# Performance work log

Hardware: AMD Instinct MI355X
Metric: run time of the kernel (lower is better)

## Reference

```python
import jax, jax.numpy as jnp
import numpy as np

B, L, H, HEADS = 4, 256, 256, 4
D = H // HEADS
NEG = jnp.float32(-2.0**32 + 1)


def setup_inputs() -> dict:
    key = jax.random.key(0)
    ks = jax.random.split(key, 16)
    inp = {
        "queries": jax.random.normal(ks[0], (B, L, H), jnp.float32),
        "keys": jax.random.normal(ks[1], (B, L, H), jnp.float32),
        "values": jax.random.normal(ks[2], (B, L, H), jnp.float32),
        "time_matrix_K": jax.random.normal(ks[3], (B, L, L, H), jnp.float32),
        "time_matrix_V": jax.random.normal(ks[4], (B, L, L, H), jnp.float32),
        "abs_pos_K": jax.random.normal(ks[5], (B, L, H), jnp.float32),
        "abs_pos_V": jax.random.normal(ks[6], (B, L, H), jnp.float32),
        "time_mask": jax.random.randint(ks[7], (B, L), 0, 2) == 1,
        "future_time_mask": jnp.triu(jnp.ones((L, L), bool), k=1),
        # linear layer params (torch Linear: y = x @ W.T + b)
        "Wq": jax.random.normal(ks[8], (H, H), jnp.float32) / np.sqrt(H),
        "bq": jax.random.normal(ks[9], (H,), jnp.float32) * 0.01,
        "Wk": jax.random.normal(ks[10], (H, H), jnp.float32) / np.sqrt(H),
        "bk": jax.random.normal(ks[11], (H,), jnp.float32) * 0.01,
        "Wv": jax.random.normal(ks[12], (H, H), jnp.float32) / np.sqrt(H),
        "bv": jax.random.normal(ks[13], (H,), jnp.float32) * 0.01,
    }
    return inp


def _split_heads(x):  # [B,L,H] -> [h,B,L,d]
    b, l, _ = x.shape
    return x.reshape(b, l, HEADS, D).transpose(2, 0, 1, 3)


def _split_heads_rel(t):  # [B,L,L,H] -> [h,B,L,L,d]
    b, l, _, _ = t.shape
    return t.reshape(b, l, l, HEADS, D).transpose(3, 0, 1, 2, 4)


def reference(queries, keys, values, time_matrix_K, time_matrix_V,
              abs_pos_K, abs_pos_V, time_mask, future_time_mask,
              Wq, bq, Wk, bk, Wv, bv):
    Q = _split_heads(queries @ Wq.T + bq)   # [h,B,L,d]
    K = _split_heads(keys @ Wk.T + bk)
    V = _split_heads(values @ Wv.T + bv)
    tK = _split_heads_rel(time_matrix_K)    # [h,B,L,L,d]
    tV = _split_heads_rel(time_matrix_V)
    pK = _split_heads(abs_pos_K)            # [h,B,L,d]
    pV = _split_heads(abs_pos_V)

    scores = jnp.einsum("hbqd,hbkd->hbqk", Q, K)
    scores += jnp.einsum("hbqd,hbkd->hbqk", Q, pK)
    scores += jnp.einsum("hbqkd,hbqd->hbqk", tK, Q)
    scores = scores / jnp.sqrt(jnp.float32(D))

    mask = time_mask[None, :, :, None] | future_time_mask[None, None, :, :]
    scores = jnp.where(mask, NEG, scores)
    attn = jax.nn.softmax(scores, axis=-1)  # [h,B,L,L]  (dropout: eval mode)

    out = jnp.einsum("hbqk,hbkd->hbqd", attn, V)
    out += jnp.einsum("hbqk,hbkd->hbqd", attn, pV)
    out += jnp.einsum("hbqk,hbqkd->hbqd", attn, tV)
    # merge heads: [h,B,L,d] -> [B,L,H]
    return out.transpose(1, 2, 0, 3).reshape(B, L, H)
```

## Files before the change

### kernel.cpp

```cpp
#include <hip/hip_runtime.h>
#include <math.h>
#include <stdint.h>

#define LSEQ 256
#define HD 256

__device__ __forceinline__ float dot4(float4 a, float4 b) {
    return a.x * b.x + a.y * b.y + a.z * b.z + a.w * b.w;
}
__device__ __forceinline__ float4 add4(float4 a, float4 b) {
    return make_float4(a.x + b.x, a.y + b.y, a.z + b.z, a.w + b.w);
}

__global__ __launch_bounds__(256) void proj_kernel(
    const float* __restrict__ queries, const float* __restrict__ keys,
    const float* __restrict__ values,
    const float* __restrict__ apK, const float* __restrict__ apV,
    const float* __restrict__ Wq, const float* __restrict__ bq,
    const float* __restrict__ Wk, const float* __restrict__ bk,
    const float* __restrict__ Wv, const float* __restrict__ bv,
    float* __restrict__ Qo, float* __restrict__ Ko, float* __restrict__ Vo)
{
    const int R = 4;
    int tid = threadIdx.x;
    int row0 = blockIdx.x * R;

    float aq[R] = {0.f, 0.f, 0.f, 0.f};
    float ak[R] = {0.f, 0.f, 0.f, 0.f};
    float av[R] = {0.f, 0.f, 0.f, 0.f};

    const float* wq = Wq + tid * HD;
    const float* wk = Wk + tid * HD;
    const float* wv = Wv + tid * HD;

    #pragma unroll 2
    for (int i = 0; i < HD; i += 4) {
        float4 wq4 = *(const float4*)(wq + i);
        float4 wk4 = *(const float4*)(wk + i);
        float4 wv4 = *(const float4*)(wv + i);
        #pragma unroll
        for (int r = 0; r < R; ++r) {
            float4 xq = *(const float4*)(queries + (row0 + r) * HD + i);
            float4 xk = *(const float4*)(keys    + (row0 + r) * HD + i);
            float4 xv = *(const float4*)(values  + (row0 + r) * HD + i);
            aq[r] += dot4(xq, wq4);
            ak[r] += dot4(xk, wk4);
            av[r] += dot4(xv, wv4);
        }
    }
    #pragma unroll
    for (int r = 0; r < R; ++r) {
        int idx = (row0 + r) * HD + tid;
        Qo[idx] = aq[r] + bq[tid];
        Ko[idx] = ak[r] + bk[tid] + apK[idx];
        Vo[idx] = av[r] + bv[tid] + apV[idx];
    }
}

__global__ __launch_bounds__(256, 4) void scores_kernel(
    const float* __restrict__ Q, const float* __restrict__ Keff,
    const float* __restrict__ tK, const int* __restrict__ tmask,
    float* __restrict__ sc_out)
{
    int bid = blockIdx.x;
    int bq = bid >> 3;
    int c = bid & 7;
    int q = bq & 255;
    int b = bq >> 8;
    int k0c = c << 5;
    if (k0c > q || tmask[bq]) return;

    int tid = threadIdx.x;
    int v = tid >> 6;
    int lane = tid & 63;
    int head = lane >> 4;
    int le4 = lane * 4;

    const float* tKr = tK + (size_t)bq * (LSEQ * HD);
    const float* Kb  = Keff + b * (LSEQ * HD);
    float4 q4 = *(const float4*)(Q + bq * HD + le4);
    int kend = min(k0c + 32, q + 1);
    float* scrow = sc_out + (size_t)(bq * 4 + head) * LSEQ;

    int k = k0c + v;
    for (; k + 12 < kend; k += 16) {
        float4 t0 = *(const float4*)(tKr + (k     ) * HD + le4);
        float4 t1 = *(const float4*)(tKr + (k +  4) * HD + le4);
        float4 t2 = *(const float4*)(tKr + (k +  8) * HD + le4);
        float4 t3 = *(const float4*)(tKr + (k + 12) * HD + le4);
        float4 c0 = *(const float4*)(Kb  + (k     ) * HD + le4);
        float4 c1 = *(const float4*)(Kb  + (k +  4) * HD + le4);
        float4 c2 = *(const float4*)(Kb  + (k +  8) * HD + le4);
        float4 c3 = *(const float4*)(Kb  + (k + 12) * HD + le4);
        float s0 = dot4(q4, add4(t0, c0));
        float s1 = dot4(q4, add4(t1, c1));
        float s2 = dot4(q4, add4(t2, c2));
        float s3 = dot4(q4, add4(t3, c3));
        #pragma unroll
        for (int off = 1; off <= 8; off <<= 1) {
            s0 += __shfl_xor(s0, off);
            s1 += __shfl_xor(s1, off);
            s2 += __shfl_xor(s2, off);
            s3 += __shfl_xor(s3, off);
        }
        if ((lane & 15) == 0) {
            scrow[k     ] = s0 * 0.125f;
            scrow[k +  4] = s1 * 0.125f;
            scrow[k +  8] = s2 * 0.125f;
            scrow[k + 12] = s3 * 0.125f;
        }
    }
    for (; k < kend; k += 4) {
        float4 t0 = *(const float4*)(tKr + k * HD + le4);
        float4 c0 = *(const float4*)(Kb  + k * HD + le4);
        float s0 = dot4(q4, add4(t0, c0));
        #pragma unroll
        for (int off = 1; off <= 8; off <<= 1)
            s0 += __shfl_xor(s0, off);
        if ((lane & 15) == 0) scrow[k] = s0 * 0.125f;
    }
}

__global__ __launch_bounds__(256, 4) void softmax_kernel(
    float* __restrict__ sc, const int* __restrict__ tmask)
{
    int bq = blockIdx.x;
    if (tmask[bq]) return;
    int q = bq & 255;
    int tid = threadIdx.x;
    int w = tid >> 6;
    int lane = tid & 63;
    float* row = sc + (size_t)(bq * 4 + w) * LSEQ;
    int k0 = lane * 4;
    float4 vv = *(const float4*)(row + k0);
    float x0 = (k0 + 0 <= q) ? vv.x : -INFINITY;
    float x1 = (k0 + 1 <= q) ? vv.y : -INFINITY;
    float x2 = (k0 + 2 <= q) ? vv.z : -INFINITY;
    float x3 = (k0 + 3 <= q) ? vv.w : -INFINITY;
    float m = fmaxf(fmaxf(x0, x1), fmaxf(x2, x3));
    #pragma unroll
    for (int off = 32; off >= 1; off >>= 1)
        m = fmaxf(m, __shfl_xor(m, off));
    float e0 = __expf(x0 - m);
    float e1 = __expf(x1 - m);
    float e2 = __expf(x2 - m);
    float e3 = __expf(x3 - m);
    float ssum = e0 + e1 + e2 + e3;
    #pragma unroll
    for (int off = 32; off >= 1; off >>= 1)
        ssum += __shfl_xor(ssum, off);
    float inv = 1.0f / ssum;
    *(float4*)(row + k0) = make_float4(e0 * inv, e1 * inv, e2 * inv, e3 * inv);
}

__global__ __launch_bounds__(256, 4) void pv_kernel(
    const float* __restrict__ Veff, const float* __restrict__ tV,
    const float* __restrict__ attn, const int* __restrict__ tmask,
    float* __restrict__ part)
{
    __shared__ float outp[4][256];

    int bid = blockIdx.x;
    int bq = bid >> 2;
    int c = bid & 3;
    int q = bq & 255;
    int b = bq >> 8;
    bool masked = tmask[bq] != 0;
    int kstart = c << 6;
    if (!masked && kstart > q) return;
    int kend = min(kstart + 64, masked ? LSEQ : q + 1);

    int tid = threadIdx.x;
    int v = tid >> 6;
    int lane = tid & 63;
    int head = lane >> 4;
    int le4 = lane * 4;

    const float* tVr = tV + (size_t)bq * (LSEQ * HD);
    const float* Vb  = Veff + b * (LSEQ * HD);
    const float* arow = attn + (size_t)(bq * 4 + head) * LSEQ;
    const float uw = 1.0f / 256.0f;

    float4 acc = make_float4(0.f, 0.f, 0.f, 0.f);
    int k = kstart + v;
    for (; k + 12 < kend; k += 16) {
        float4 t0 = *(const float4*)(tVr + (k     ) * HD + le4);
        float4 t1 = *(const float4*)(tVr + (k +  4) * HD + le4);
        float4 t2 = *(const float4*)(tVr + (k +  8) * HD + le4);
        float4 t3 = *(const float4*)(tVr + (k + 12) * HD + le4);
        float4 v0 = *(const float4*)(Vb  + (k     ) * HD + le4);
        float4 v1 = *(const float4*)(Vb  + (k +  4) * HD + le4);
        float4 v2 = *(const float4*)(Vb  + (k +  8) * HD + le4);
        float4 v3 = *(const float4*)(Vb  + (k + 12) * HD + le4);
        float a0 = masked ? uw : arow[k     ];
        float a1 = masked ? uw : arow[k +  4];
        float a2 = masked ? uw : arow[k +  8];
        float a3 = masked ? uw : arow[k + 12];
        acc.x += a0 * (t0.x + v0.x) + a1 * (t1.x + v1.x)
               + a2 * (t2.x + v2.x) + a3 * (t3.x + v3.x);
        acc.y += a0 * (t0.y + v0.y) + a1 * (t1.y + v1.y)
               + a2 * (t2.y + v2.y) + a3 * (t3.y + v3.y);
        acc.z += a0 * (t0.z + v0.z) + a1 * (t1.z + v1.z)
               + a2 * (t2.z + v2.z) + a3 * (t3.z + v3.z);
        acc.w += a0 * (t0.w + v0.w) + a1 * (t1.w + v1.w)
               + a2 * (t2.w + v2.w) + a3 * (t3.w + v3.w);
    }
    for (; k < kend; k += 4) {
        float4 t0 = *(const float4*)(tVr + k * HD + le4);
        float4 v0 = *(const float4*)(Vb  + k * HD + le4);
        float a0 = masked ? uw : arow[k];
        acc.x += a0 * (t0.x + v0.x);
        acc.y += a0 * (t0.y + v0.y);
        acc.z += a0 * (t0.z + v0.z);
        acc.w += a0 * (t0.w + v0.w);
    }
    *(float4*)(&outp[v][le4]) = acc;
    __syncthreads();
    float o = outp[0][tid] + outp[1][tid] + outp[2][tid] + outp[3][tid];
    part[((size_t)((c << 10) | bq)) * HD + tid] = o;
}

__global__ __launch_bounds__(256) void reduce_kernel(
    const float* __restrict__ part, const int* __restrict__ tmask,
    float* __restrict__ out)
{
    int bq = blockIdx.x;
    int q = bq & 255;
    int tid = threadIdx.x;
    int nch = tmask[bq] ? 4 : ((q >> 6) + 1);
    float o = 0.f;
    for (int c = 0; c < nch; ++c)
        o += part[((size_t)((c << 10) | bq)) * HD + tid];
    out[(size_t)bq * HD + tid] = o;
}

extern "C" void kernel_launch(void* const* d_in, const int* in_sizes, int n_in,
                              void* d_out, int out_size, void* d_ws, size_t ws_size,
                              hipStream_t stream) {
    const float* queries = (const float*)d_in[0];
    const float* keys    = (const float*)d_in[1];
    const float* values  = (const float*)d_in[2];
    const float* tK      = (const float*)d_in[3];
    const float* tV      = (const float*)d_in[4];
    const float* apK     = (const float*)d_in[5];
    const float* apV     = (const float*)d_in[6];
    const int*   tmask   = (const int*)d_in[7];
    const float* Wq = (const float*)d_in[9];
    const float* bq = (const float*)d_in[10];
    const float* Wk = (const float*)d_in[11];
    const float* bk = (const float*)d_in[12];
    const float* Wv = (const float*)d_in[13];
    const float* bv = (const float*)d_in[14];

    float* ws = (float*)d_ws;
    float* Qo     = ws;
    float* Ko     = ws + 262144;
    float* Vo     = ws + 524288;
    float* scores = ws + 786432;
    float* partb  = ws + 1835008;
    float* out = (float*)d_out;

    proj_kernel<<<256, 256, 0, stream>>>(queries, keys, values, apK, apV,
                                         Wq, bq, Wk, bk, Wv, bv, Qo, Ko, Vo);
    scores_kernel<<<8192, 256, 0, stream>>>(Qo, Ko, tK, tmask, scores);
    softmax_kernel<<<1024, 256, 0, stream>>>(scores, tmask);
    pv_kernel<<<4096, 256, 0, stream>>>(Vo, tV, scores, tmask, partb);
    reduce_kernel<<<1024, 256, 0, stream>>>(partb, tmask, out);
}
```

Measured before the change: 113.5 us.

## Use nontemporal loads for time matrices and contiguous per-wave key ranges

Streams the large tK/tV tensors with nontemporal loads so they do not pollute cache that K/V reuse needs. Each wave now handles a contiguous 16-key range instead of interleaved keys, which allows float4 stores of scores and float4 loads of attention weights. The scores kernel is re-gridded to 64-key chunks with half as many blocks, and the occupancy hints are dropped from the launch bounds. Contiguous ranges may give less even load balance near the causal boundary.

```diff
diff --git a/kernel.cpp b/kernel.cpp
--- a/kernel.cpp
+++ b/kernel.cpp
@@ -5,11 +5,17 @@
 #define LSEQ 256
 #define HD 256
 
+typedef float floatx4 __attribute__((ext_vector_type(4)));
+
 __device__ __forceinline__ float dot4(float4 a, float4 b) {
     return a.x * b.x + a.y * b.y + a.z * b.z + a.w * b.w;
 }
 __device__ __forceinline__ float4 add4(float4 a, float4 b) {
     return make_float4(a.x + b.x, a.y + b.y, a.z + b.z, a.w + b.w);
+}
+__device__ __forceinline__ float4 ldnt4(const float* p) {
+    floatx4 r = __builtin_nontemporal_load((const floatx4*)p);
+    return make_float4(r.x, r.y, r.z, r.w);
 }
 
 __global__ __launch_bounds__(256) void proj_kernel(
@@ -57,17 +63,17 @@
     }
 }
 
-__global__ __launch_bounds__(256, 4) void scores_kernel(
+__global__ __launch_bounds__(256) void scores_kernel(
     const float* __restrict__ Q, const float* __restrict__ Keff,
     const float* __restrict__ tK, const int* __restrict__ tmask,
     float* __restrict__ sc_out)
 {
     int bid = blockIdx.x;
-    int bq = bid >> 3;
-    int c = bid & 7;
+    int bq = bid >> 2;
+    int c = bid & 3;
     int q = bq & 255;
     int b = bq >> 8;
-    int k0c = c << 5;
+    int k0c = c << 6;
     if (k0c > q || tmask[bq]) return;
 
     int tid = threadIdx.x;
@@ -79,19 +85,21 @@
     const float* tKr = tK + (size_t)bq * (LSEQ * HD);
     const float* Kb  = Keff + b * (LSEQ * HD);
     float4 q4 = *(const float4*)(Q + bq * HD + le4);
-    int kend = min(k0c + 32, q + 1);
     float* scrow = sc_out + (size_t)(bq * 4 + head) * LSEQ;
 
-    int k = k0c + v;
-    for (; k + 12 < kend; k += 16) {
-        float4 t0 = *(const float4*)(tKr + (k     ) * HD + le4);
-        float4 t1 = *(const float4*)(tKr + (k +  4) * HD + le4);
-        float4 t2 = *(const float4*)(tKr + (k +  8) * HD + le4);
-        float4 t3 = *(const float4*)(tKr + (k + 12) * HD + le4);
-        float4 c0 = *(const float4*)(Kb  + (k     ) * HD + le4);
-        float4 c1 = *(const float4*)(Kb  + (k +  4) * HD + le4);
-        float4 c2 = *(const float4*)(Kb  + (k +  8) * HD + le4);
-        float4 c3 = *(const float4*)(Kb  + (k + 12) * HD + le4);
+    int r0 = k0c + v * 16;
+    int rend = min(r0 + 16, q + 1);
+
+    int k = r0;
+    for (; k + 3 < rend; k += 4) {
+        float4 t0 = ldnt4(tKr + (k    ) * HD + le4);
+        float4 t1 = ldnt4(tKr + (k + 1) * HD + le4);
+        float4 t2 = ldnt4(tKr + (k + 2) * HD + le4);
+        float4 t3 = ldnt4(tKr + (k + 3) * HD + le4);
+        float4 c0 = *(const float4*)(Kb + (k    ) * HD + le4);
+        float4 c1 = *(const float4*)(Kb + (k + 1) * HD + le4);
+        float4 c2 = *(const float4*)(Kb + (k + 2) * HD + le4);
+        float4 c3 = *(const float4*)(Kb + (k + 3) * HD + le4);
         float s0 = dot4(q4, add4(t0, c0));
         float s1 = dot4(q4, add4(t1, c1));
         float s2 = dot4(q4, add4(t2, c2));
@@ -103,16 +111,13 @@
             s2 += __shfl_xor(s2, off);
             s3 += __shfl_xor(s3, off);
         }
-        if ((lane & 15) == 0) {
-            scrow[k     ] = s0 * 0.125f;
-            scrow[k +  4] = s1 * 0.125f;
-            scrow[k +  8] = s2 * 0.125f;
-            scrow[k + 12] = s3 * 0.125f;
-        }
-    }
-    for (; k < kend; k += 4) {
-        float4 t0 = *(const float4*)(tKr + k * HD + le4);
-        float4 c0 = *(const float4*)(Kb  + k * HD + le4);
+        if ((lane & 15) == 0)
+            *(float4*)(scrow + k) = make_float4(s0 * 0.125f, s1 * 0.125f,
+                                                s2 * 0.125f, s3 * 0.125f);
+    }
+    for (; k < rend; ++k) {
+        float4 t0 = ldnt4(tKr + k * HD + le4);
+        float4 c0 = *(const float4*)(Kb + k * HD + le4);
         float s0 = dot4(q4, add4(t0, c0));
         #pragma unroll
         for (int off = 1; off <= 8; off <<= 1)
@@ -121,7 +126,7 @@
     }
 }
 
-__global__ __launch_bounds__(256, 4) void softmax_kernel(
+__global__ __launch_bounds__(256) void softmax_kernel(
     float* __restrict__ sc, const int* __restrict__ tmask)
 {
     int bq = blockIdx.x;
@@ -153,7 +158,7 @@
     *(float4*)(row + k0) = make_float4(e0 * inv, e1 * inv, e2 * inv, e3 * inv);
 }
 
-__global__ __launch_bounds__(256, 4) void pv_kernel(
+__global__ __launch_bounds__(256) void pv_kernel(
     const float* __restrict__ Veff, const float* __restrict__ tV,
     const float* __restrict__ attn, const int* __restrict__ tmask,
     float* __restrict__ part)
@@ -168,7 +173,7 @@
     bool masked = tmask[bq] != 0;
     int kstart = c << 6;
     if (!masked && kstart > q) return;
-    int kend = min(kstart + 64, masked ? LSEQ : q + 1);
+    int kendc = min(kstart + 64, masked ? LSEQ : q + 1);
 
     int tid = threadIdx.x;
     int v = tid >> 6;
@@ -181,33 +186,35 @@
     const float* arow = attn + (size_t)(bq * 4 + head) * LSEQ;
     const float uw = 1.0f / 256.0f;
 
+    int r0 = kstart + v * 16;
+    int rend = min(r0 + 16, kendc);
+
     float4 acc = make_float4(0.f, 0.f, 0.f, 0.f);
-    int k = kstart + v;
-    for (; k + 12 < kend; k += 16) {
-        float4 t0 = *(const float4*)(tVr + (k     ) * HD + le4);
-        float4 t1 = *(const float4*)(tVr + (k +  4) * HD + le4);
-        float4 t2 = *(const float4*)(tVr + (k +  8) * HD + le4);
-        float4 t3 = *(const float4*)(tVr + (k + 12) * HD + le4);
-        float4 v0 = *(const float4*)(Vb  + (k     ) * HD + le4);
-        float4 v1 = *(const float4*)(Vb  + (k +  4) * HD + le4);
-        float4 v2 = *(const float4*)(Vb  + (k +  8) * HD + le4);
-        float4 v3 = *(const float4*)(Vb  + (k + 12) * HD + le4);
-        float a0 = masked ? uw : arow[k     ];
-        float a1 = masked ? uw : arow[k +  4];
-        float a2 = masked ? uw : arow[k +  8];
-        float a3 = masked ? uw : arow[k + 12];
-        acc.x += a0 * (t0.x + v0.x) + a1 * (t1.x + v1.x)
-               + a2 * (t2.x + v2.x) + a3 * (t3.x + v3.x);
-        acc.y += a0 * (t0.y + v0.y) + a1 * (t1.y + v1.y)
-               + a2 * (t2.y + v2.y) + a3 * (t3.y + v3.y);
-        acc.z += a0 * (t0.z + v0.z) + a1 * (t1.z + v1.z)
-               + a2 * (t2.z + v2.z) + a3 * (t3.z + v3.z);
-        acc.w += a0 * (t0.w + v0.w) + a1 * (t1.w + v1.w)
-               + a2 * (t2.w + v2.w) + a3 * (t3.w + v3.w);
-    }
-    for (; k < kend; k += 4) {
-        float4 t0 = *(const float4*)(tVr + k * HD + le4);
-        float4 v0 = *(const float4*)(Vb  + k * HD + le4);
+    int k = r0;
+    for (; k + 3 < rend; k += 4) {
+        float4 t0 = ldnt4(tVr + (k    ) * HD + le4);
+        float4 t1 = ldnt4(tVr + (k + 1) * HD + le4);
+        float4 t2 = ldnt4(tVr + (k + 2) * HD + le4);
+        float4 t3 = ldnt4(tVr + (k + 3) * HD + le4);
+        float4 v0 = *(const float4*)(Vb + (k    ) * HD + le4);
+        float4 v1 = *(const float4*)(Vb + (k + 1) * HD + le4);
+        float4 v2 = *(const float4*)(Vb + (k + 2) * HD + le4);
+        float4 v3 = *(const float4*)(Vb + (k + 3) * HD + le4);
+        float4 a4;
+        if (masked) a4 = make_float4(uw, uw, uw, uw);
+        else        a4 = *(const float4*)(arow + k);
+        acc.x += a4.x * (t0.x + v0.x) + a4.y * (t1.x + v1.x)
+               + a4.z * (t2.x + v2.x) + a4.w * (t3.x + v3.x);
+        acc.y += a4.x * (t0.y + v0.y) + a4.y * (t1.y + v1.y)
+               + a4.z * (t2.y + v2.y) + a4.w * (t3.y + v3.y);
+        acc.z += a4.x * (t0.z + v0.z) + a4.y * (t1.z + v1.z)
+               + a4.z * (t2.z + v2.z) + a4.w * (t3.z + v3.z);
+        acc.w += a4.x * (t0.w + v0.w) + a4.y * (t1.w + v1.w)
+               + a4.z * (t2.w + v2.w) + a4.w * (t3.w + v3.w);
+    }
+    for (; k < rend; ++k) {
+        float4 t0 = ldnt4(tVr + k * HD + le4);
+        float4 v0 = *(const float4*)(Vb + k * HD + le4);
         float a0 = masked ? uw : arow[k];
         acc.x += a0 * (t0.x + v0.x);
         acc.y += a0 * (t0.y + v0.y);
@@ -262,7 +269,7 @@
 
     proj_kernel<<<256, 256, 0, stream>>>(queries, keys, values, apK, apV,
                                          Wq, bq, Wk, bk, Wv, bv, Qo, Ko, Vo);
-    scores_kernel<<<8192, 256, 0, stream>>>(Qo, Ko, tK, tmask, scores);
+    scores_kernel<<<4096, 256, 0, stream>>>(Qo, Ko, tK, tmask, scores);
     softmax_kernel<<<1024, 256, 0, stream>>>(scores, tmask);
     pv_kernel<<<4096, 256, 0, stream>>>(Vo, tV, scores, tmask, partb);
     reduce_kernel<<<1024, 256, 0, stream>>>(partb, tmask, out);
```

Result: faster. 108.6 us (-4.3%).
